# Kernel optimization log

Hardware: AMD Instinct MI355X
Metric: run time of the kernel (lower is better)

## Reference

```python
import jax, jax.numpy as jnp
import numpy as np

N_NODES = 100000
N_EDGES = 1600000
D = 128


def setup_inputs() -> dict:
    key = jax.random.key(0)
    k1, k2, k3 = jax.random.split(key, 3)
    x = jax.random.normal(k1, (N_NODES, D), dtype=jnp.float32)
    edge_index = jax.random.randint(k2, (2, N_EDGES), 0, N_NODES, dtype=jnp.int64)
    weight = jax.random.normal(k3, (D, D), dtype=jnp.float32) * (1.0 / np.sqrt(D))
    bias = jnp.zeros((D,), dtype=jnp.float32)
    return {"x": x, "edge_index": edge_index, "weight": weight, "bias": bias}


def reference(x, edge_index, weight, bias):
    # Eval-mode forward: dropout(p=0.5, training=False) is identity.
    N = x.shape[0]
    row, col = edge_index[0], edge_index[1]  # source -> target

    # gcn_norm: add self loops (weight 1), symmetric normalization
    loop = jnp.arange(N, dtype=edge_index.dtype)
    full_row = jnp.concatenate([row, loop])
    full_col = jnp.concatenate([col, loop])
    ew = jnp.ones(full_row.shape[0], dtype=x.dtype)
    deg = jax.ops.segment_sum(ew, full_col, num_segments=N)
    deg_inv_sqrt = jnp.where(deg > 0, jax.lax.rsqrt(jnp.maximum(deg, 1e-12)), 0.0)
    norm = deg_inv_sqrt[full_row] * ew * deg_inv_sqrt[full_col]  # [E+N]

    # linear transform then gather-scale-scatter aggregation
    h = x @ weight.T  # [N, D]
    msgs = h[full_row] * norm[:, None]  # [E+N, D]
    out = jax.ops.segment_sum(msgs, full_col, num_segments=N)
    out = out + bias
    return jax.nn.relu(out)
```

## Files before the change

kernel.cpp:

```cpp
#include <hip/hip_runtime.h>

#define N_NODES 100000
#define N_EDGES 1600000
#define D 128
#define N_STRIPS (N_NODES / 32)

#define BSH   8
#define NBKT  391
#define P_BLK 512
#define EPB   (N_EDGES / P_BLK)

typedef __bf16 bf16x4 __attribute__((ext_vector_type(4)));
typedef __bf16 bf16x8 __attribute__((ext_vector_type(8)));
typedef float  f32x4  __attribute__((ext_vector_type(4)));

__global__ __launch_bounds__(1024) void k_prep(const int* __restrict__ col,
                                               const float4* __restrict__ w4,
                                               int* __restrict__ bhist,
                                               bf16x4* __restrict__ wb4) {
    int tid = threadIdx.x, b = blockIdx.x;
    if (b == P_BLK) {
        for (int i = tid; i < (D * D) / 4; i += 1024) {
            float4 u = w4[i];
            bf16x4 p;
            p[0] = (__bf16)u.x; p[1] = (__bf16)u.y;
            p[2] = (__bf16)u.z; p[3] = (__bf16)u.w;
            wb4[i] = p;
        }
        return;
    }
    __shared__ int lh[NBKT];
    if (tid < NBKT) lh[tid] = 0;
    __syncthreads();
    int e0 = b * EPB;
    for (int e = e0 + tid; e < e0 + EPB; e += 1024)
        atomicAdd(&lh[col[e] >> BSH], 1);
    __syncthreads();
    if (tid < NBKT) bhist[tid * P_BLK + b] = lh[tid];
}

__global__ __launch_bounds__(512) void k_bscan(int* __restrict__ bhist,
                                               int* __restrict__ gtot) {
    __shared__ int buf[512];
    int k = blockIdx.x, t = threadIdx.x;
    int v = bhist[k * P_BLK + t];
    buf[t] = v;
    __syncthreads();
    for (int off = 1; off < 512; off <<= 1) {
        int u = (t >= off) ? buf[t - off] : 0;
        __syncthreads();
        buf[t] += u;
        __syncthreads();
    }
    bhist[k * P_BLK + t] = buf[t] - v;
    if (t == 511) gtot[k] = buf[511];
}

__global__ __launch_bounds__(512) void k_gscan(const int* __restrict__ gtot,
                                               int* __restrict__ gstart) {
    __shared__ int buf[512];
    int t = threadIdx.x;
    int v = (t < NBKT) ? gtot[t] : 0;
    buf[t] = v;
    __syncthreads();
    for (int off = 1; off < 512; off <<= 1) {
        int u = (t >= off) ? buf[t - off] : 0;
        __syncthreads();
        buf[t] += u;
        __syncthreads();
    }
    if (t < NBKT) gstart[t] = buf[t] - v;
}

__global__ __launch_bounds__(1024) void k_cscatter(const int* __restrict__ row,
                                                   const int* __restrict__ col,
                                                   const int* __restrict__ bhist,
                                                   const int* __restrict__ gstart,
                                                   unsigned* __restrict__ grec) {
    __shared__ int cur[NBKT];
    int b = blockIdx.x, t = threadIdx.x;
    if (t < NBKT) cur[t] = gstart[t] + bhist[t * P_BLK + b];
    __syncthreads();
    int e0 = b * EPB;
    for (int e = e0 + t; e < e0 + EPB; e += 1024) {
        int c = col[e];
        unsigned rec = ((unsigned)row[e] << BSH) | (unsigned)(c & ((1 << BSH) - 1));
        int pos = atomicAdd(&cur[c >> BSH], 1);
        grec[pos] = rec;
    }
}

__global__ __launch_bounds__(1024) void k_fine(const unsigned* __restrict__ grec,
                                               const int* __restrict__ gtot,
                                               const int* __restrict__ gstart,
                                               int* __restrict__ deg,
                                               float* __restrict__ dis,
                                               int* __restrict__ start,
                                               int* __restrict__ srcs) {
    __shared__ int fh[256];
    __shared__ int fsc[256];
    int b = blockIdx.x;
    int tid = threadIdx.x;
    int cnt = gtot[b];
    int gs = gstart[b];
    if (tid < 256) fh[tid] = 0;
    __syncthreads();
    for (int i = tid; i < cnt; i += 1024)
        atomicAdd(&fh[grec[gs + i] & 255], 1);
    __syncthreads();
    int v = 0;
    if (tid < 256) { v = fh[tid]; fsc[tid] = v; }
    __syncthreads();
    for (int off = 1; off < 256; off <<= 1) {
        int u = 0;
        if (tid < 256 && tid >= off) u = fsc[tid - off];
        __syncthreads();
        if (tid < 256) fsc[tid] += u;
        __syncthreads();
    }
    if (tid < 256) {
        int excl = fsc[tid] - v;
        int node = (b << BSH) + tid;
        if (node < N_NODES) {
            deg[node]   = v;
            dis[node]   = rsqrtf((float)v + 1.0f);
            start[node] = gs + excl;
        }
        fh[tid] = excl;
    }
    __syncthreads();
    for (int i = tid; i < cnt; i += 1024) {
        unsigned r = grec[gs + i];
        int pos = atomicAdd(&fh[r & 255], 1);
        srcs[gs + pos] = (int)((r >> BSH) << 8);
    }
}

__global__ __launch_bounds__(256) void k_hx(const float* __restrict__ x,
                                            const __bf16* __restrict__ wb,
                                            const float* __restrict__ dis,
                                            __bf16* __restrict__ hb) {
    int wave = threadIdx.x >> 6;
    int lane = threadIdx.x & 63;
    int strip = blockIdx.x * 4 + wave;
    if (strip >= N_STRIPS) return;
    int m0 = strip * 32;
    int l15 = lane & 15;
    int kq  = lane >> 4;

    bf16x8 a[2][4];
    #pragma unroll
    for (int mt = 0; mt < 2; ++mt) {
        const float* ap = x + (size_t)(m0 + mt * 16 + l15) * D + kq * 8;
        #pragma unroll
        for (int ks = 0; ks < 4; ++ks) {
            float4 lo = *(const float4*)(ap + ks * 32);
            float4 hi = *(const float4*)(ap + ks * 32 + 4);
            bf16x8 t;
            t[0] = (__bf16)lo.x; t[1] = (__bf16)lo.y;
            t[2] = (__bf16)lo.z; t[3] = (__bf16)lo.w;
            t[4] = (__bf16)hi.x; t[5] = (__bf16)hi.y;
            t[6] = (__bf16)hi.z; t[7] = (__bf16)hi.w;
            a[mt][ks] = t;
        }
    }

    f32x4 acc[2][8] = {};
    #pragma unroll
    for (int ks = 0; ks < 4; ++ks) {
        #pragma unroll
        for (int nt = 0; nt < 8; ++nt) {
            bf16x8 b = *(const bf16x8*)(wb + (size_t)(nt * 16 + l15) * D + ks * 32 + kq * 8);
            acc[0][nt] = __builtin_amdgcn_mfma_f32_16x16x32_bf16(a[0][ks], b, acc[0][nt], 0, 0, 0);
            acc[1][nt] = __builtin_amdgcn_mfma_f32_16x16x32_bf16(a[1][ks], b, acc[1][nt], 0, 0, 0);
        }
    }

    float dsv[2][4];
    #pragma unroll
    for (int mt = 0; mt < 2; ++mt)
        #pragma unroll
        for (int r = 0; r < 4; ++r)
            dsv[mt][r] = dis[m0 + mt * 16 + kq * 4 + r];

    #pragma unroll
    for (int nt = 0; nt < 8; ++nt) {
        int colj = nt * 16 + l15;
        #pragma unroll
        for (int mt = 0; mt < 2; ++mt) {
            #pragma unroll
            for (int r = 0; r < 4; ++r) {
                int rowi = m0 + mt * 16 + kq * 4 + r;
                hb[(size_t)rowi * D + colj] = (__bf16)(acc[mt][nt][r] * dsv[mt][r]);
            }
        }
    }
}

__global__ __launch_bounds__(256) void k_aggregate(const int* __restrict__ srcs,
                                                   const int* __restrict__ start,
                                                   const int* __restrict__ deg,
                                                   const __bf16* __restrict__ hb,
                                                   const float* __restrict__ dis,
                                                   const float* __restrict__ bias,
                                                   float* __restrict__ out) {
    int node = (blockIdx.x * 256 + threadIdx.x) >> 6;
    int lane = threadIdx.x & 63;
    if (node >= N_NODES) return;
    int li   = lane & 31;
    int half = lane >> 5;
    int s = start[node];
    int n = deg[node];
    float dc = dis[node];
    const unsigned char* hbase = (const unsigned char*)hb;
    size_t boff = (size_t)li * 8;

    float acc0 = 0.f, acc1 = 0.f, acc2 = 0.f, acc3 = 0.f;

    for (int base = 0; base < n; base += 64) {
        int m = n - base; if (m > 64) m = 64;
        int src_l = (lane < m) ? srcs[s + base + lane] : 0;
        int i = 0;
        for (; i + 16 <= m; i += 16) {
            int sv[8]; uint2 av[8];
            #pragma unroll
            for (int j = 0; j < 8; ++j)
                sv[j] = __shfl(src_l, i + 2 * j + half);
            #pragma unroll
            for (int j = 0; j < 8; ++j)
                av[j] = *(const uint2*)(hbase + ((size_t)sv[j] + boff));
            #pragma unroll
            for (int j = 0; j < 8; ++j) {
                acc0 += __uint_as_float(av[j].x << 16);
                acc1 += __uint_as_float(av[j].x & 0xFFFF0000u);
                acc2 += __uint_as_float(av[j].y << 16);
                acc3 += __uint_as_float(av[j].y & 0xFFFF0000u);
            }
        }
        for (; i + 2 <= m; i += 2) {
            int sj = __shfl(src_l, i + half);
            uint2 a = *(const uint2*)(hbase + ((size_t)sj + boff));
            acc0 += __uint_as_float(a.x << 16);
            acc1 += __uint_as_float(a.x & 0xFFFF0000u);
            acc2 += __uint_as_float(a.y << 16);
            acc3 += __uint_as_float(a.y & 0xFFFF0000u);
        }
        if (i < m) {
            int sj = __shfl(src_l, i);
            if (half == 0) {
                uint2 a = *(const uint2*)(hbase + ((size_t)sj + boff));
                acc0 += __uint_as_float(a.x << 16);
                acc1 += __uint_as_float(a.x & 0xFFFF0000u);
                acc2 += __uint_as_float(a.y << 16);
                acc3 += __uint_as_float(a.y & 0xFFFF0000u);
            }
        }
    }

    acc0 += __shfl_xor(acc0, 32);
    acc1 += __shfl_xor(acc1, 32);
    acc2 += __shfl_xor(acc2, 32);
    acc3 += __shfl_xor(acc3, 32);

    if (half == 0) {
        uint2 a = *(const uint2*)(hbase + ((size_t)node * 256 + boff));
        acc0 += __uint_as_float(a.x << 16);
        acc1 += __uint_as_float(a.x & 0xFFFF0000u);
        acc2 += __uint_as_float(a.y << 16);
        acc3 += __uint_as_float(a.y & 0xFFFF0000u);

        float4 b4 = *(const float4*)(bias + li * 4);
        float4 r;
        r.x = fmaxf(acc0 * dc + b4.x, 0.f);
        r.y = fmaxf(acc1 * dc + b4.y, 0.f);
        r.z = fmaxf(acc2 * dc + b4.z, 0.f);
        r.w = fmaxf(acc3 * dc + b4.w, 0.f);
        *(float4*)(out + (size_t)node * D + li * 4) = r;
    }
}

extern "C" void kernel_launch(void* const* d_in, const int* in_sizes, int n_in,
                              void* d_out, int out_size, void* d_ws, size_t ws_size,
                              hipStream_t stream) {
    const float* x    = (const float*)d_in[0];
    const int*   ei   = (const int*)d_in[1];
    const float* w    = (const float*)d_in[2];
    const float* bias = (const float*)d_in[3];
    float* out = (float*)d_out;

    char* ws = (char*)d_ws;
    int*      deg    = (int*)ws;              ws += N_NODES * 4;
    float*    dis    = (float*)ws;            ws += N_NODES * 4;
    int*      start  = (int*)ws;              ws += N_NODES * 4;
    int*      bhist  = (int*)ws;              ws += (size_t)NBKT * P_BLK * 4;
    int*      gtot   = (int*)ws;              ws += 512 * 4;
    int*      gstart = (int*)ws;              ws += 512 * 4;
    __bf16*   wb     = (__bf16*)ws;           ws += D * D * 2;
    unsigned* grec   = (unsigned*)ws;         ws += (size_t)N_EDGES * 4;
    int*      srcs   = (int*)ws;              ws += (size_t)N_EDGES * 4;
    __bf16*   hb     = (__bf16*)ws;

    const int* row = ei;
    const int* col = ei + N_EDGES;

    k_prep     <<<P_BLK + 1, 1024, 0, stream>>>(col, (const float4*)w, bhist, (bf16x4*)wb);
    k_bscan    <<<NBKT, 512, 0, stream>>>(bhist, gtot);
    k_gscan    <<<1, 512, 0, stream>>>(gtot, gstart);
    k_cscatter <<<P_BLK, 1024, 0, stream>>>(row, col, bhist, gstart, grec);
    k_fine     <<<NBKT, 1024, 0, stream>>>(grec, gtot, gstart, deg, dis, start, srcs);
    k_hx       <<<(N_STRIPS + 3) / 4, 256, 0, stream>>>(x, wb, dis, hb);
    k_aggregate<<<(N_NODES * 64 + 255) / 256, 256, 0, stream>>>(srcs, start, deg, hb, dis, bias, out);
}
```

Measured before the change: 227.7 us.

## Replace multi-pass CSR build with fixed-capacity bucket arenas and fewer kernels

```diff
diff --git a/kernel.cpp b/kernel.cpp
--- a/kernel.cpp
+++ b/kernel.cpp
@@ -7,139 +7,20 @@
 
 #define BSH   8
 #define NBKT  391
-#define P_BLK 512
-#define EPB   (N_EDGES / P_BLK)
-
-typedef __bf16 bf16x4 __attribute__((ext_vector_type(4)));
+#define ARENA 5120
+#define SC_BLK 256
+#define EPS   (N_EDGES / SC_BLK)
+
 typedef __bf16 bf16x8 __attribute__((ext_vector_type(8)));
 typedef float  f32x4  __attribute__((ext_vector_type(4)));
 
-__global__ __launch_bounds__(1024) void k_prep(const int* __restrict__ col,
-                                               const float4* __restrict__ w4,
-                                               int* __restrict__ bhist,
-                                               bf16x4* __restrict__ wb4) {
-    int tid = threadIdx.x, b = blockIdx.x;
-    if (b == P_BLK) {
-        for (int i = tid; i < (D * D) / 4; i += 1024) {
-            float4 u = w4[i];
-            bf16x4 p;
-            p[0] = (__bf16)u.x; p[1] = (__bf16)u.y;
-            p[2] = (__bf16)u.z; p[3] = (__bf16)u.w;
-            wb4[i] = p;
-        }
-        return;
-    }
-    __shared__ int lh[NBKT];
-    if (tid < NBKT) lh[tid] = 0;
-    __syncthreads();
-    int e0 = b * EPB;
-    for (int e = e0 + tid; e < e0 + EPB; e += 1024)
-        atomicAdd(&lh[col[e] >> BSH], 1);
-    __syncthreads();
-    if (tid < NBKT) bhist[tid * P_BLK + b] = lh[tid];
-}
-
-__global__ __launch_bounds__(512) void k_bscan(int* __restrict__ bhist,
-                                               int* __restrict__ gtot) {
-    __shared__ int buf[512];
-    int k = blockIdx.x, t = threadIdx.x;
-    int v = bhist[k * P_BLK + t];
-    buf[t] = v;
-    __syncthreads();
-    for (int off = 1; off < 512; off <<= 1) {
-        int u = (t >= off) ? buf[t - off] : 0;
-        __syncthreads();
-        buf[t] += u;
-        __syncthreads();
-    }
-    bhist[k * P_BLK + t] = buf[t] - v;
-    if (t == 511) gtot[k] = buf[511];
-}
-
-__global__ __launch_bounds__(512) void k_gscan(const int* __restrict__ gtot,
-                                               int* __restrict__ gstart) {
-    __shared__ int buf[512];
-    int t = threadIdx.x;
-    int v = (t < NBKT) ? gtot[t] : 0;
-    buf[t] = v;
-    __syncthreads();
-    for (int off = 1; off < 512; off <<= 1) {
-        int u = (t >= off) ? buf[t - off] : 0;
-        __syncthreads();
-        buf[t] += u;
-        __syncthreads();
-    }
-    if (t < NBKT) gstart[t] = buf[t] - v;
-}
-
-__global__ __launch_bounds__(1024) void k_cscatter(const int* __restrict__ row,
-                                                   const int* __restrict__ col,
-                                                   const int* __restrict__ bhist,
-                                                   const int* __restrict__ gstart,
-                                                   unsigned* __restrict__ grec) {
-    __shared__ int cur[NBKT];
-    int b = blockIdx.x, t = threadIdx.x;
-    if (t < NBKT) cur[t] = gstart[t] + bhist[t * P_BLK + b];
-    __syncthreads();
-    int e0 = b * EPB;
-    for (int e = e0 + t; e < e0 + EPB; e += 1024) {
-        int c = col[e];
-        unsigned rec = ((unsigned)row[e] << BSH) | (unsigned)(c & ((1 << BSH) - 1));
-        int pos = atomicAdd(&cur[c >> BSH], 1);
-        grec[pos] = rec;
-    }
-}
-
-__global__ __launch_bounds__(1024) void k_fine(const unsigned* __restrict__ grec,
-                                               const int* __restrict__ gtot,
-                                               const int* __restrict__ gstart,
-                                               int* __restrict__ deg,
-                                               float* __restrict__ dis,
-                                               int* __restrict__ start,
-                                               int* __restrict__ srcs) {
-    __shared__ int fh[256];
-    __shared__ int fsc[256];
-    int b = blockIdx.x;
-    int tid = threadIdx.x;
-    int cnt = gtot[b];
-    int gs = gstart[b];
-    if (tid < 256) fh[tid] = 0;
-    __syncthreads();
-    for (int i = tid; i < cnt; i += 1024)
-        atomicAdd(&fh[grec[gs + i] & 255], 1);
-    __syncthreads();
-    int v = 0;
-    if (tid < 256) { v = fh[tid]; fsc[tid] = v; }
-    __syncthreads();
-    for (int off = 1; off < 256; off <<= 1) {
-        int u = 0;
-        if (tid < 256 && tid >= off) u = fsc[tid - off];
-        __syncthreads();
-        if (tid < 256) fsc[tid] += u;
-        __syncthreads();
-    }
-    if (tid < 256) {
-        int excl = fsc[tid] - v;
-        int node = (b << BSH) + tid;
-        if (node < N_NODES) {
-            deg[node]   = v;
-            dis[node]   = rsqrtf((float)v + 1.0f);
-            start[node] = gs + excl;
-        }
-        fh[tid] = excl;
-    }
-    __syncthreads();
-    for (int i = tid; i < cnt; i += 1024) {
-        unsigned r = grec[gs + i];
-        int pos = atomicAdd(&fh[r & 255], 1);
-        srcs[gs + pos] = (int)((r >> BSH) << 8);
-    }
-}
-
 __global__ __launch_bounds__(256) void k_hx(const float* __restrict__ x,
-                                            const __bf16* __restrict__ wb,
-                                            const float* __restrict__ dis,
-                                            __bf16* __restrict__ hb) {
+                                            const float* __restrict__ w,
+                                            __bf16* __restrict__ hb,
+                                            int* __restrict__ gcnt) {
+    if (blockIdx.x == 0) {
+        for (int i = threadIdx.x; i < NBKT; i += 256) gcnt[i] = 0;
+    }
     int wave = threadIdx.x >> 6;
     int lane = threadIdx.x & 63;
     int strip = blockIdx.x * 4 + wave;
@@ -170,18 +51,18 @@
     for (int ks = 0; ks < 4; ++ks) {
         #pragma unroll
         for (int nt = 0; nt < 8; ++nt) {
-            bf16x8 b = *(const bf16x8*)(wb + (size_t)(nt * 16 + l15) * D + ks * 32 + kq * 8);
-            acc[0][nt] = __builtin_amdgcn_mfma_f32_16x16x32_bf16(a[0][ks], b, acc[0][nt], 0, 0, 0);
-            acc[1][nt] = __builtin_amdgcn_mfma_f32_16x16x32_bf16(a[1][ks], b, acc[1][nt], 0, 0, 0);
-        }
-    }
-
-    float dsv[2][4];
-    #pragma unroll
-    for (int mt = 0; mt < 2; ++mt)
-        #pragma unroll
-        for (int r = 0; r < 4; ++r)
-            dsv[mt][r] = dis[m0 + mt * 16 + kq * 4 + r];
+            const float* bp = w + (size_t)(nt * 16 + l15) * D + ks * 32 + kq * 8;
+            float4 lo = *(const float4*)bp;
+            float4 hi = *(const float4*)(bp + 4);
+            bf16x8 bfr;
+            bfr[0] = (__bf16)lo.x; bfr[1] = (__bf16)lo.y;
+            bfr[2] = (__bf16)lo.z; bfr[3] = (__bf16)lo.w;
+            bfr[4] = (__bf16)hi.x; bfr[5] = (__bf16)hi.y;
+            bfr[6] = (__bf16)hi.z; bfr[7] = (__bf16)hi.w;
+            acc[0][nt] = __builtin_amdgcn_mfma_f32_16x16x32_bf16(a[0][ks], bfr, acc[0][nt], 0, 0, 0);
+            acc[1][nt] = __builtin_amdgcn_mfma_f32_16x16x32_bf16(a[1][ks], bfr, acc[1][nt], 0, 0, 0);
+        }
+    }
 
     #pragma unroll
     for (int nt = 0; nt < 8; ++nt) {
@@ -191,13 +72,92 @@
             #pragma unroll
             for (int r = 0; r < 4; ++r) {
                 int rowi = m0 + mt * 16 + kq * 4 + r;
-                hb[(size_t)rowi * D + colj] = (__bf16)(acc[mt][nt][r] * dsv[mt][r]);
-            }
-        }
-    }
-}
-
-__global__ __launch_bounds__(256) void k_aggregate(const int* __restrict__ srcs,
+                hb[(size_t)rowi * D + colj] = (__bf16)acc[mt][nt][r];
+            }
+        }
+    }
+}
+
+__global__ __launch_bounds__(1024) void k_scatter(const int* __restrict__ row,
+                                                  const int* __restrict__ col,
+                                                  int* __restrict__ gcnt,
+                                                  unsigned* __restrict__ arena) {
+    __shared__ int rc[EPS];
+    __shared__ int cc[EPS];
+    __shared__ int lcnt[NBKT];
+    __shared__ int lbase[NBKT];
+    int b = blockIdx.x, t = threadIdx.x;
+    if (t < NBKT) lcnt[t] = 0;
+    __syncthreads();
+    int e0 = b * EPS;
+    for (int i = t; i < EPS; i += 1024) {
+        int r = row[e0 + i], c = col[e0 + i];
+        rc[i] = r; cc[i] = c;
+        atomicAdd(&lcnt[c >> BSH], 1);
+    }
+    __syncthreads();
+    if (t < NBKT) lbase[t] = atomicAdd(&gcnt[t], lcnt[t]);
+    __syncthreads();
+    if (t < NBKT) lcnt[t] = 0;
+    __syncthreads();
+    for (int i = t; i < EPS; i += 1024) {
+        int c = cc[i];
+        int k = c >> BSH;
+        int idx = lbase[k] + atomicAdd(&lcnt[k], 1);
+        if (idx < ARENA)
+            arena[(size_t)k * ARENA + idx] = ((unsigned)rc[i] << BSH) | (unsigned)(c & ((1 << BSH) - 1));
+    }
+}
+
+__global__ __launch_bounds__(1024) void k_fine(unsigned* __restrict__ arena,
+                                               const int* __restrict__ gcnt,
+                                               int* __restrict__ deg,
+                                               float* __restrict__ dis,
+                                               int* __restrict__ start) {
+    __shared__ unsigned cache[ARENA];
+    __shared__ int fh[256];
+    __shared__ int fsc[256];
+    int b = blockIdx.x;
+    int tid = threadIdx.x;
+    int cnt = gcnt[b]; if (cnt > ARENA) cnt = ARENA;
+    int gs = b * ARENA;
+    if (tid < 256) fh[tid] = 0;
+    __syncthreads();
+    for (int i = tid; i < cnt; i += 1024) {
+        unsigned r = arena[gs + i];
+        cache[i] = r;
+        atomicAdd(&fh[r & 255], 1);
+    }
+    __syncthreads();
+    int v = 0;
+    if (tid < 256) { v = fh[tid]; fsc[tid] = v; }
+    __syncthreads();
+    for (int off = 1; off < 256; off <<= 1) {
+        int u = 0;
+        if (tid < 256 && tid >= off) u = fsc[tid - off];
+        __syncthreads();
+        if (tid < 256) fsc[tid] += u;
+        __syncthreads();
+    }
+    if (tid < 256) {
+        int excl = fsc[tid] - v;
+        int node = (b << BSH) + tid;
+        if (node < N_NODES) {
+            deg[node]   = v;
+            dis[node]   = rsqrtf((float)v + 1.0f);
+            start[node] = gs + excl;
+        }
+        fh[tid] = excl;
+    }
+    __syncthreads();
+    for (int i = tid; i < cnt; i += 1024) {
+        unsigned r = cache[i];
+        int pos = atomicAdd(&fh[r & 255], 1);
+        arena[gs + pos] = (r >> BSH) << 8;
+    }
+}
+
+__global__ __launch_bounds__(256) void k_aggregate(const unsigned* __restrict__ srcs,
                                                    const int* __restrict__ start,
                                                    const int* __restrict__ deg,
                                                    const __bf16* __restrict__ hb,
@@ -219,40 +179,49 @@
 
     for (int base = 0; base < n; base += 64) {
         int m = n - base; if (m > 64) m = 64;
-        int src_l = (lane < m) ? srcs[s + base + lane] : 0;
+        int   src_l = 0;
+        float nr_l  = 0.f;
+        if (lane < m) {
+            src_l = (int)srcs[s + base + lane];
+            nr_l  = dis[src_l >> 8];
+        }
         int i = 0;
         for (; i + 16 <= m; i += 16) {
-            int sv[8]; uint2 av[8];
-            #pragma unroll
-            for (int j = 0; j < 8; ++j)
+            int sv[8]; float nv[8]; uint2 av[8];
+            #pragma unroll
+            for (int j = 0; j < 8; ++j) {
                 sv[j] = __shfl(src_l, i + 2 * j + half);
+                nv[j] = __shfl(nr_l, i + 2 * j + half);
+            }
             #pragma unroll
             for (int j = 0; j < 8; ++j)
                 av[j] = *(const uint2*)(hbase + ((size_t)sv[j] + boff));
             #pragma unroll
             for (int j = 0; j < 8; ++j) {
-                acc0 += __uint_as_float(av[j].x << 16);
-                acc1 += __uint_as_float(av[j].x & 0xFFFF0000u);
-                acc2 += __uint_as_float(av[j].y << 16);
-                acc3 += __uint_as_float(av[j].y & 0xFFFF0000u);
+                acc0 += __uint_as_float(av[j].x << 16) * nv[j];
+                acc1 += __uint_as_float(av[j].x & 0xFFFF0000u) * nv[j];
+                acc2 += __uint_as_float(av[j].y << 16) * nv[j];
+                acc3 += __uint_as_float(av[j].y & 0xFFFF0000u) * nv[j];
             }
         }
         for (; i + 2 <= m; i += 2) {
-            int sj = __shfl(src_l, i + half);
+            int   sj = __shfl(src_l, i + half);
+            float nj = __shfl(nr_l, i + half);
             uint2 a = *(const uint2*)(hbase + ((size_t)sj + boff));
-            acc0 += __uint_as_float(a.x << 16);
-            acc1 += __uint_as_float(a.x & 0xFFFF0000u);
-            acc2 += __uint_as_float(a.y << 16);
-            acc3 += __uint_as_float(a.y & 0xFFFF0000u);
+            acc0 += __uint_as_float(a.x << 16) * nj;
+            acc1 += __uint_as_float(a.x & 0xFFFF0000u) * nj;
+            acc2 += __uint_as_float(a.y << 16) * nj;
+            acc3 += __uint_as_float(a.y & 0xFFFF0000u) * nj;
         }
         if (i < m) {
-            int sj = __shfl(src_l, i);
+            int   sj = __shfl(src_l, i);
+            float nj = __shfl(nr_l, i);
             if (half == 0) {
                 uint2 a = *(const uint2*)(hbase + ((size_t)sj + boff));
-                acc0 += __uint_as_float(a.x << 16);
-                acc1 += __uint_as_float(a.x & 0xFFFF0000u);
-                acc2 += __uint_as_float(a.y << 16);
-                acc3 += __uint_as_float(a.y & 0xFFFF0000u);
+                acc0 += __uint_as_float(a.x << 16) * nj;
+                acc1 += __uint_as_float(a.x & 0xFFFF0000u) * nj;
+                acc2 += __uint_as_float(a.y << 16) * nj;
+                acc3 += __uint_as_float(a.y & 0xFFFF0000u) * nj;
             }
         }
     }
@@ -264,10 +233,10 @@
 
     if (half == 0) {
         uint2 a = *(const uint2*)(hbase + ((size_t)node * 256 + boff));
-        acc0 += __uint_as_float(a.x << 16);
-        acc1 += __uint_as_float(a.x & 0xFFFF0000u);
-        acc2 += __uint_as_float(a.y << 16);
-        acc3 += __uint_as_float(a.y & 0xFFFF0000u);
+        acc0 += __uint_as_float(a.x << 16) * dc;
+        acc1 += __uint_as_float(a.x & 0xFFFF0000u) * dc;
+        acc2 += __uint_as_float(a.y << 16) * dc;
+        acc3 += __uint_as_float(a.y & 0xFFFF0000u) * dc;
 
         float4 b4 = *(const float4*)(bias + li * 4);
         float4 r;
@@ -292,22 +261,15 @@
     int*      deg    = (int*)ws;              ws += N_NODES * 4;
     float*    dis    = (float*)ws;            ws += N_NODES * 4;
     int*      start  = (int*)ws;              ws += N_NODES * 4;
-    int*      bhist  = (int*)ws;              ws += (size_t)NBKT * P_BLK * 4;
-    int*      gtot   = (int*)ws;              ws += 512 * 4;
-    int*      gstart = (int*)ws;              ws += 512 * 4;
-    __bf16*   wb     = (__bf16*)ws;           ws += D * D * 2;
-    unsigned* grec   = (unsigned*)ws;         ws += (size_t)N_EDGES * 4;
-    int*      srcs   = (int*)ws;              ws += (size_t)N_EDGES * 4;
+    int*      gcnt   = (int*)ws;              ws += 512 * 4;
+    unsigned* arena  = (unsigned*)ws;         ws += (size_t)NBKT * ARENA * 4;
     __bf16*   hb     = (__bf16*)ws;
 
     const int* row = ei;
     const int* col = ei + N_EDGES;
 
-    k_prep     <<<P_BLK + 1, 1024, 0, stream>>>(col, (const float4*)w, bhist, (bf16x4*)wb);
-    k_bscan    <<<NBKT, 512, 0, stream>>>(bhist, gtot);
-    k_gscan    <<<1, 512, 0, stream>>>(gtot, gstart);
-    k_cscatter <<<P_BLK, 1024, 0, stream>>>(row, col, bhist, gstart, grec);
-    k_fine     <<<NBKT, 1024, 0, stream>>>(grec, gtot, gstart, deg, dis, start, srcs);
-    k_hx       <<<(N_STRIPS + 3) / 4, 256, 0, stream>>>(x, wb, dis, hb);
-    k_aggregate<<<(N_NODES * 64 + 255) / 256, 256, 0, stream>>>(srcs, start, deg, hb, dis, bias, out);
-}
+    k_hx       <<<(N_STRIPS + 3) / 4, 256, 0, stream>>>(x, w, hb, gcnt);
+    k_scatter  <<<SC_BLK, 1024, 0, stream>>>(row, col, gcnt, arena);
+    k_fine     <<<NBKT, 1024, 0, stream>>>(arena, gcnt, deg, dis, start);
+    k_aggregate<<<(N_NODES * 64 + 255) / 256, 256, 0, stream>>>(arena, start, deg, hb, dis, bias, out);
+}
```

Measured after the change: 235.9 us. 1.04x slower.

## Locally sort edges in LDS before coarse bucket scatter, widen buckets to 512 nodes

Applied to the files above, without the earlier changes.

```diff
diff --git a/kernel.cpp b/kernel.cpp
--- a/kernel.cpp
+++ b/kernel.cpp
@@ -5,8 +5,8 @@
 #define D 128
 #define N_STRIPS (N_NODES / 32)
 
-#define BSH   8
-#define NBKT  391
+#define BSH   9
+#define NBKT  196
 #define P_BLK 512
 #define EPB   (N_EDGES / P_BLK)
 
@@ -56,14 +56,14 @@
     if (t == 511) gtot[k] = buf[511];
 }
 
-__global__ __launch_bounds__(512) void k_gscan(const int* __restrict__ gtot,
+__global__ __launch_bounds__(256) void k_gscan(const int* __restrict__ gtot,
                                                int* __restrict__ gstart) {
-    __shared__ int buf[512];
+    __shared__ int buf[256];
     int t = threadIdx.x;
     int v = (t < NBKT) ? gtot[t] : 0;
     buf[t] = v;
     __syncthreads();
-    for (int off = 1; off < 512; off <<= 1) {
+    for (int off = 1; off < 256; off <<= 1) {
         int u = (t >= off) ? buf[t - off] : 0;
         __syncthreads();
         buf[t] += u;
@@ -77,17 +77,52 @@
                                                    const int* __restrict__ bhist,
                                                    const int* __restrict__ gstart,
                                                    unsigned* __restrict__ grec) {
-    __shared__ int cur[NBKT];
+    __shared__ int      rec[EPB];
+    __shared__ unsigned short kb[EPB];
+    __shared__ int      srt[EPB];
+    __shared__ int      dofp[EPB];
+    __shared__ int      lh[256];
+    __shared__ int      sc[256];
+    __shared__ int      cur[256];
+    __shared__ int      dofk[256];
     int b = blockIdx.x, t = threadIdx.x;
-    if (t < NBKT) cur[t] = gstart[t] + bhist[t * P_BLK + b];
+    if (t < 256) lh[t] = 0;
     __syncthreads();
     int e0 = b * EPB;
-    for (int e = e0 + t; e < e0 + EPB; e += 1024) {
-        int c = col[e];
-        unsigned rec = ((unsigned)row[e] << BSH) | (unsigned)(c & ((1 << BSH) - 1));
-        int pos = atomicAdd(&cur[c >> BSH], 1);
-        grec[pos] = rec;
-    }
+    for (int i = t; i < EPB; i += 1024) {
+        int r = row[e0 + i], c = col[e0 + i];
+        int k = c >> BSH;
+        rec[i] = (r << BSH) | (c & ((1 << BSH) - 1));
+        kb[i]  = (unsigned short)k;
+        atomicAdd(&lh[k], 1);
+    }
+    __syncthreads();
+    int v = 0;
+    if (t < 256) { v = lh[t]; sc[t] = v; }
+    __syncthreads();
+    for (int off = 1; off < 256; off <<= 1) {
+        int u = 0;
+        if (t < 256 && t >= off) u = sc[t - off];
+        __syncthreads();
+        if (t < 256) sc[t] += u;
+        __syncthreads();
+    }
+    if (t < 256) {
+        int excl = sc[t] - v;
+        sc[t]  = excl;
+        cur[t] = 0;
+        dofk[t] = (t < NBKT) ? (gstart[t] + bhist[t * P_BLK + b] - excl) : 0;
+    }
+    __syncthreads();
+    for (int i = t; i < EPB; i += 1024) {
+        int k = kb[i];
+        int p = sc[k] + atomicAdd(&cur[k], 1);
+        srt[p]  = rec[i];
+        dofp[p] = dofk[k];
+    }
+    __syncthreads();
+    for (int i = t; i < EPB; i += 1024)
+        grec[i + dofp[i]] = (unsigned)srt[i];
 }
 
 __global__ __launch_bounds__(1024) void k_fine(const unsigned* __restrict__ grec,
@@ -97,28 +132,28 @@
                                                float* __restrict__ dis,
                                                int* __restrict__ start,
                                                int* __restrict__ srcs) {
-    __shared__ int fh[256];
-    __shared__ int fsc[256];
+    __shared__ int fh[512];
+    __shared__ int fsc[512];
     int b = blockIdx.x;
     int tid = threadIdx.x;
     int cnt = gtot[b];
     int gs = gstart[b];
-    if (tid < 256) fh[tid] = 0;
+    if (tid < 512) fh[tid] = 0;
     __syncthreads();
     for (int i = tid; i < cnt; i += 1024)
-        atomicAdd(&fh[grec[gs + i] & 255], 1);
+        atomicAdd(&fh[grec[gs + i] & 511], 1);
     __syncthreads();
     int v = 0;
-    if (tid < 256) { v = fh[tid]; fsc[tid] = v; }
-    __syncthreads();
-    for (int off = 1; off < 256; off <<= 1) {
+    if (tid < 512) { v = fh[tid]; fsc[tid] = v; }
+    __syncthreads();
+    for (int off = 1; off < 512; off <<= 1) {
         int u = 0;
-        if (tid < 256 && tid >= off) u = fsc[tid - off];
-        __syncthreads();
-        if (tid < 256) fsc[tid] += u;
-        __syncthreads();
-    }
-    if (tid < 256) {
+        if (tid < 512 && tid >= off) u = fsc[tid - off];
+        __syncthreads();
+        if (tid < 512) fsc[tid] += u;
+        __syncthreads();
+    }
+    if (tid < 512) {
         int excl = fsc[tid] - v;
         int node = (b << BSH) + tid;
         if (node < N_NODES) {
@@ -131,7 +166,7 @@
     __syncthreads();
     for (int i = tid; i < cnt; i += 1024) {
         unsigned r = grec[gs + i];
-        int pos = atomicAdd(&fh[r & 255], 1);
+        int pos = atomicAdd(&fh[r & 511], 1);
         srcs[gs + pos] = (int)((r >> BSH) << 8);
     }
 }
@@ -305,7 +340,7 @@
 
     k_prep     <<<P_BLK + 1, 1024, 0, stream>>>(col, (const float4*)w, bhist, (bf16x4*)wb);
     k_bscan    <<<NBKT, 512, 0, stream>>>(bhist, gtot);
-    k_gscan    <<<1, 512, 0, stream>>>(gtot, gstart);
+    k_gscan    <<<1, 256, 0, stream>>>(gtot, gstart);
     k_cscatter <<<P_BLK, 1024, 0, stream>>>(row, col, bhist, gstart, grec);
     k_fine     <<<NBKT, 1024, 0, stream>>>(grec, gtot, gstart, deg, dis, start, srcs);
     k_hx       <<<(N_STRIPS + 3) / 4, 256, 0, stream>>>(x, wb, dis, hb);
```

Result: no change. 224.7 us (-1.3%).
